# Optimization experiments

Measured on AMD Instinct MI355X. Metric: run time of the kernel, lower is better.

The kernel has to match this reference:

```python
import jax, jax.numpy as jnp
import numpy as np

B, S, D, H, HD, F = 2, 2048, 2048, 16, 128, 8192
EPS = 1e-6
NEG_INF = -1e10


def rmsnorm(x, scale, eps=EPS):
    # T5 LayerNorm: no centering, mean of squares, learned scale
    x = x.astype(jnp.float32)
    mean2 = jnp.mean(jnp.square(x), axis=-1, keepdims=True)
    return x * jax.lax.rsqrt(mean2 + eps) * scale


def setup_inputs() -> dict:
    key = jax.random.key(0)
    ks = jax.random.split(key, 10)
    sd = 0.02
    return {
        "x": jax.random.normal(ks[0], (B, S, D), jnp.float32),
        "ln1_scale": jnp.ones((D,), jnp.float32),
        "wq": jax.random.normal(ks[1], (D, H, HD), jnp.float32) * sd,
        "wk": jax.random.normal(ks[2], (D, H, HD), jnp.float32) * sd,
        "wv": jax.random.normal(ks[3], (D, H, HD), jnp.float32) * sd,
        "qln_scale": jnp.ones((HD,), jnp.float32),
        "kln_scale": jnp.ones((HD,), jnp.float32),
        "wo": jax.random.normal(ks[4], (H, HD, D), jnp.float32) * sd,
        "ln2_scale": jnp.ones((D,), jnp.float32),
        "wi0": jax.random.normal(ks[5], (D, F), jnp.float32) * sd,
        "wi1": jax.random.normal(ks[6], (D, F), jnp.float32) * sd,
        "wout": jax.random.normal(ks[7], (F, D), jnp.float32) * sd,
    }


def reference(x, ln1_scale, wq, wk, wv, qln_scale, kln_scale, wo, ln2_scale, wi0, wi1, wout):
    # ---- pre-attention RMSNorm ----
    lnx = rmsnorm(x, ln1_scale)                                  # [B,S,D]
    # ---- QKV projections (DenseGeneral D -> (H,HD)) ----
    q = jnp.einsum("bsd,dhk->bshk", lnx, wq)                      # [B,S,H,HD]
    k = jnp.einsum("bsd,dhk->bshk", lnx, wk)
    v = jnp.einsum("bsd,dhk->bshk", lnx, wv)
    # ---- fused per-head QK LayerNorm ----
    q = rmsnorm(q, qln_scale)
    k = rmsnorm(k, kln_scale)
    # ---- attention scores + causal bias + softmax ----
    logits = jnp.einsum("bqhd,bkhd->bhqk", q, k)                  # [B,H,S,S]
    causal = jnp.tril(jnp.ones((S, S), bool))
    bias = jnp.where(causal, 0.0, NEG_INF).astype(logits.dtype)  # [S,S]
    probs = jax.nn.softmax(logits + bias[None, None])             # [B,H,S,S]
    # ---- weighted values + output projection ----
    attn = jnp.einsum("bhqk,bkhd->bqhd", probs, v)                # [B,S,H,HD]
    attn_out = jnp.einsum("bqhd,hdm->bqm", attn, wo)              # [B,S,D]
    inter = x + attn_out
    # ---- pre-MLP RMSNorm + gated MLP (silu * linear) ----
    h = rmsnorm(inter, ln2_scale)
    g = jax.nn.silu(h @ wi0) * (h @ wi1)                          # [B,S,F]
    mlp_out = g @ wout                                            # [B,S,D]
    return inter + mlp_out
```

## Files before the change

### kernel.cpp

```cpp
#include <hip/hip_runtime.h>

typedef unsigned short u16;
typedef unsigned int u32;
typedef __attribute__((ext_vector_type(8))) short bf16x8;
typedef __attribute__((ext_vector_type(2))) float f32x2;
typedef __attribute__((ext_vector_type(4))) float f32x4;
typedef __attribute__((ext_vector_type(4))) u32 u32x4;

#define DEV __device__ __forceinline__

DEV u16 f2bf(float x) {
    u32 u = __builtin_bit_cast(u32, x);
    u += 0x7fffu + ((u >> 16) & 1u);
    return (u16)(u >> 16);
}
DEV float bf2f(u16 b) {
    u32 u = ((u32)b) << 16;
    return __builtin_bit_cast(float, u);
}

#define MFMA16(a, b, c) __builtin_amdgcn_mfma_f32_16x16x32_bf16((a), (b), (c), 0, 0, 0)

#define GLL16(gp, lp)                                                      \
    __builtin_amdgcn_global_load_lds(                                      \
        (const __attribute__((address_space(1))) u32*)(const void*)(gp),   \
        (__attribute__((address_space(3))) u32*)(void*)(lp), 16, 0, 0)

__global__ void fillsent(float* __restrict__ out, int n, float val)
{
    for (int i = blockIdx.x * blockDim.x + threadIdx.x; i < n; i += gridDim.x * blockDim.x)
        out[i] = val;
}

__global__ void wtrans(const float* __restrict__ in, u16* __restrict__ out, int K, int N)
{
    __shared__ u16 t[64][65];
    const int n0 = blockIdx.x * 64, k0 = blockIdx.y * 64, tid = threadIdx.x;
    for (int i = tid; i < 4096; i += 256) {
        int r = i >> 6, c = i & 63;
        t[r][c] = f2bf(in[(size_t)(k0 + r) * N + n0 + c]);
    }
    __syncthreads();
    for (int i = tid; i < 4096; i += 256) {
        int r = i >> 6, c = i & 63;
        out[(size_t)(n0 + r) * K + k0 + c] = t[c][r];
    }
}

__global__ void wtrans_split(const float* __restrict__ in, u16* __restrict__ ohi,
                             u16* __restrict__ olo, int K, int N)
{
    __shared__ float t[64][65];
    const int n0 = blockIdx.x * 64, k0 = blockIdx.y * 64, tid = threadIdx.x;
    for (int i = tid; i < 4096; i += 256) {
        int r = i >> 6, c = i & 63;
        t[r][c] = in[(size_t)(k0 + r) * N + n0 + c];
    }
    __syncthreads();
    for (int i = tid; i < 4096; i += 256) {
        int r = i >> 6, c = i & 63;
        float v = t[c][r];
        u16 h = f2bf(v);
        size_t idx = (size_t)(n0 + r) * K + k0 + c;
        ohi[idx] = h;
        olo[idx] = f2bf(v - bf2f(h));
    }
}

__global__ void vtrans(const u16* __restrict__ in, u16* __restrict__ out)
{
    __shared__ u16 t[64][65];
    const int d0 = blockIdx.x * 64, s0 = blockIdx.y * 64, bh = blockIdx.z, tid = threadIdx.x;
    const u16* ip = in + (size_t)bh * 2048 * 128;
    u16* op = out + (size_t)bh * 128 * 2048;
    for (int i = tid; i < 4096; i += 256) {
        int r = i >> 6, c = i & 63;
        t[r][c] = ip[(size_t)(s0 + r) * 128 + d0 + c];
    }
    __syncthreads();
    for (int i = tid; i < 4096; i += 256) {
        int r = i >> 6, c = i & 63;
        op[(size_t)(d0 + r) * 2048 + s0 + c] = t[c][r];
    }
}

__global__ __launch_bounds__(256) void rmsnorm_d(const float* __restrict__ in,
                                                 const float* __restrict__ sc,
                                                 u16* __restrict__ out)
{
    __shared__ float red[4];
    const int row = blockIdx.x, tid = threadIdx.x;
    const float* p = in + (size_t)row * 2048 + tid * 8;
    f32x4 a = *(const f32x4*)p;
    f32x4 b = *(const f32x4*)(p + 4);
    float ss = a[0]*a[0] + a[1]*a[1] + a[2]*a[2] + a[3]*a[3]
             + b[0]*b[0] + b[1]*b[1] + b[2]*b[2] + b[3]*b[3];
    for (int d = 1; d < 64; d <<= 1) ss += __shfl_xor(ss, d, 64);
    if ((tid & 63) == 0) red[tid >> 6] = ss;
    __syncthreads();
    float rs = rsqrtf((red[0] + red[1] + red[2] + red[3]) * (1.0f / 2048.0f) + 1e-6f);
    const float* s = sc + tid * 8;
    u32x4 ov;
#pragma unroll
    for (int i = 0; i < 2; ++i) {
        f32x4 v = i ? b : a;
#pragma unroll
        for (int j = 0; j < 2; ++j) {
            float v0 = v[j * 2] * rs * s[i * 4 + j * 2];
            float v1 = v[j * 2 + 1] * rs * s[i * 4 + j * 2 + 1];
            ov[i * 2 + j] = (u32)f2bf(v0) | ((u32)f2bf(v1) << 16);
        }
    }
    *(u32x4*)(out + (size_t)row * 2048 + tid * 8) = ov;
}

__global__ __launch_bounds__(256) void rmsnorm_split(const float* __restrict__ in,
                                                     const float* __restrict__ sc,
                                                     u16* __restrict__ ohi,
                                                     u16* __restrict__ olo)
{
    __shared__ float red[4];
    const int row = blockIdx.x, tid = threadIdx.x;
    const float* p = in + (size_t)row * 2048 + tid * 8;
    f32x4 a = *(const f32x4*)p;
    f32x4 b = *(const f32x4*)(p + 4);
    float ss = a[0]*a[0] + a[1]*a[1] + a[2]*a[2] + a[3]*a[3]
             + b[0]*b[0] + b[1]*b[1] + b[2]*b[2] + b[3]*b[3];
    for (int d = 1; d < 64; d <<= 1) ss += __shfl_xor(ss, d, 64);
    if ((tid & 63) == 0) red[tid >> 6] = ss;
    __syncthreads();
    float rs = rsqrtf((red[0] + red[1] + red[2] + red[3]) * (1.0f / 2048.0f) + 1e-6f);
    const float* s = sc + tid * 8;
    u32x4 oh, ol;
#pragma unroll
    for (int i = 0; i < 2; ++i) {
        f32x4 v = i ? b : a;
#pragma unroll
        for (int j = 0; j < 2; ++j) {
            float v0 = v[j * 2] * rs * s[i * 4 + j * 2];
            float v1 = v[j * 2 + 1] * rs * s[i * 4 + j * 2 + 1];
            u16 h0 = f2bf(v0), h1 = f2bf(v1);
            u16 l0 = f2bf(v0 - bf2f(h0)), l1 = f2bf(v1 - bf2f(h1));
            oh[i * 2 + j] = (u32)h0 | ((u32)h1 << 16);
            ol[i * 2 + j] = (u32)l0 | ((u32)l1 << 16);
        }
    }
    *(u32x4*)(ohi + (size_t)row * 2048 + tid * 8) = oh;
    *(u32x4*)(olo + (size_t)row * 2048 + tid * 8) = ol;
}

template <int EPI>
__global__ __launch_bounds__(256, 2)
void gemm_bt_k(const u16* __restrict__ A, const u16* __restrict__ Bt,
               float* __restrict__ outf, u16* __restrict__ outb,
               const float* __restrict__ resf, int M, int N, int K)
{
    __shared__ u16 As[128 * 64];
    __shared__ u16 Bs[128 * 64];
    const int tid = threadIdx.x, w = tid >> 6, l = tid & 63;
    const int lr = l & 15, lg = l >> 4;
    const int m0 = blockIdx.y * 128, n0 = blockIdx.x * 128;
    const int wr = (w >> 1) * 64, wc = (w & 1) * 64;
    f32x4 acc[4][4] = {};
    int prow[4], pcol[4];
#pragma unroll
    for (int j = 0; j < 4; ++j) {
        int p = (j * 4 + w) * 1024 + l * 16;
        prow[j] = p >> 7;
        pcol[j] = (p ^ ((prow[j] & 7) << 4)) & 127;
    }
    const char* Ab = (const char*)A;
    const char* Bb = (const char*)Bt;
    const size_t ldb = (size_t)K * 2;
    const int nkt = K / 64;
    for (int kt = 0; kt < nkt; ++kt) {
#pragma unroll
        for (int j = 0; j < 4; ++j) {
            GLL16(Ab + (size_t)(m0 + prow[j]) * ldb + kt * 128 + pcol[j], (char*)As + (j * 4 + w) * 1024);
            GLL16(Bb + (size_t)(n0 + prow[j]) * ldb + kt * 128 + pcol[j], (char*)Bs + (j * 4 + w) * 1024);
        }
        __syncthreads();
#pragma unroll
        for (int kc = 0; kc < 2; ++kc) {
            bf16x8 af[4], bf[4];
#pragma unroll
            for (int f = 0; f < 4; ++f) {
                int ra = wr + f * 16 + lr;
                af[f] = *(const bf16x8*)((const char*)As + ((ra * 128 + kc * 64 + lg * 16) ^ ((ra & 7) << 4)));
                int rb = wc + f * 16 + lr;
                bf[f] = *(const bf16x8*)((const char*)Bs + ((rb * 128 + kc * 64 + lg * 16) ^ ((rb & 7) << 4)));
            }
#pragma unroll
            for (int mf = 0; mf < 4; ++mf)
#pragma unroll
                for (int nf = 0; nf < 4; ++nf)
                    acc[mf][nf] = MFMA16(af[mf], bf[nf], acc[mf][nf]);
        }
        __syncthreads();
    }
#pragma unroll
    for (int mf = 0; mf < 4; ++mf) {
#pragma unroll
        for (int nf = 0; nf < 4; ++nf) {
#pragma unroll
            for (int r = 0; r < 4; ++r) {
                int m = m0 + wr + mf * 16 + lg * 4 + r;
                int n = n0 + wc + nf * 16 + lr;
                float v = acc[mf][nf][r];
                if constexpr (EPI == 0) {
                    outb[(((m >> 11) * 16 + (n >> 7)) << 18) + ((m & 2047) << 7) + (n & 127)] = f2bf(v);
                } else {
                    size_t idx = (size_t)m * N + n;
                    outf[idx] = v + resf[idx];
                }
            }
        }
    }
}

__global__ __launch_bounds__(256, 2)
void gemm3(const u16* __restrict__ Ahi, const u16* __restrict__ Alo,
           const u16* __restrict__ Bhi, const u16* __restrict__ Blo,
           const float* __restrict__ sc,
           u16* __restrict__ ohi, u16* __restrict__ olo, int M, int N, int K)
{
    __shared__ u16 Ah[128 * 64];
    __shared__ u16 Al[128 * 64];
    __shared__ u16 Bh[128 * 64];
    __shared__ u16 Bl[128 * 64];
    __shared__ float ssq[128][2];
    const int tid = threadIdx.x, w = tid >> 6, l = tid & 63;
    const int lr = l & 15, lg = l >> 4;
    const int m0 = blockIdx.y * 128, n0 = blockIdx.x * 128;
    const int wr = (w >> 1) * 64, wc = (w & 1) * 64;
    f32x4 acc[4][4] = {};
    int prow[4], pcol[4];
#pragma unroll
    for (int j = 0; j < 4; ++j) {
        int p = (j * 4 + w) * 1024 + l * 16;
        prow[j] = p >> 7;
        pcol[j] = (p ^ ((prow[j] & 7) << 4)) & 127;
    }
    const size_t ldb = (size_t)K * 2;
    const int nkt = K / 64;
    for (int kt = 0; kt < nkt; ++kt) {
#pragma unroll
        for (int j = 0; j < 4; ++j) {
            size_t ao = (size_t)(m0 + prow[j]) * ldb + kt * 128 + pcol[j];
            size_t bo = (size_t)(n0 + prow[j]) * ldb + kt * 128 + pcol[j];
            GLL16((const char*)Ahi + ao, (char*)Ah + (j * 4 + w) * 1024);
            GLL16((const char*)Alo + ao, (char*)Al + (j * 4 + w) * 1024);
            GLL16((const char*)Bhi + bo, (char*)Bh + (j * 4 + w) * 1024);
            GLL16((const char*)Blo + bo, (char*)Bl + (j * 4 + w) * 1024);
        }
        __syncthreads();
#pragma unroll
        for (int kc = 0; kc < 2; ++kc) {
            bf16x8 ahf[4], alf[4], bhf[4], blf[4];
#pragma unroll
            for (int f = 0; f < 4; ++f) {
                int ra = wr + f * 16 + lr;
                int oa = (ra * 128 + kc * 64 + lg * 16) ^ ((ra & 7) << 4);
                ahf[f] = *(const bf16x8*)((const char*)Ah + oa);
                alf[f] = *(const bf16x8*)((const char*)Al + oa);
                int rb = wc + f * 16 + lr;
                int ob = (rb * 128 + kc * 64 + lg * 16) ^ ((rb & 7) << 4);
                bhf[f] = *(const bf16x8*)((const char*)Bh + ob);
                blf[f] = *(const bf16x8*)((const char*)Bl + ob);
            }
#pragma unroll
            for (int mf = 0; mf < 4; ++mf)
#pragma unroll
                for (int nf = 0; nf < 4; ++nf) {
                    acc[mf][nf] = MFMA16(ahf[mf], bhf[nf], acc[mf][nf]);
                    acc[mf][nf] = MFMA16(ahf[mf], blf[nf], acc[mf][nf]);
                    acc[mf][nf] = MFMA16(alf[mf], bhf[nf], acc[mf][nf]);
                }
        }
        __syncthreads();
    }
    float sp[4][4];
#pragma unroll
    for (int mf = 0; mf < 4; ++mf)
#pragma unroll
        for (int r = 0; r < 4; ++r) {
            float s = 0.0f;
#pragma unroll
            for (int nf = 0; nf < 4; ++nf) { float v = acc[mf][nf][r]; s += v * v; }
            s += __shfl_xor(s, 1, 64); s += __shfl_xor(s, 2, 64);
            s += __shfl_xor(s, 4, 64); s += __shfl_xor(s, 8, 64);
            sp[mf][r] = s;
        }
    if (lr == 0) {
#pragma unroll
        for (int mf = 0; mf < 4; ++mf)
#pragma unroll
            for (int r = 0; r < 4; ++r)
                ssq[wr + mf * 16 + lg * 4 + r][w & 1] = sp[mf][r];
    }
    __syncthreads();
    const int head = n0 >> 7;
#pragma unroll
    for (int mf = 0; mf < 4; ++mf)
#pragma unroll
        for (int r = 0; r < 4; ++r) {
            int mloc = wr + mf * 16 + lg * 4 + r;
            int m = m0 + mloc;
            float rs = rsqrtf((ssq[mloc][0] + ssq[mloc][1]) * (1.0f / 128.0f) + 1e-6f);
            size_t base = (((size_t)(m >> 11) * 16 + head) << 18) + ((size_t)(m & 2047) << 7);
#pragma unroll
            for (int nf = 0; nf < 4; ++nf) {
                int hd = wc + nf * 16 + lr;
                float v = acc[mf][nf][r] * rs * sc[hd];
                u16 hv = f2bf(v);
                ohi[base + hd] = hv;
                olo[base + hd] = f2bf(v - bf2f(hv));
            }
        }
}

__global__ __launch_bounds__(256, 2)
void gemm_up(const u16* __restrict__ A, const u16* __restrict__ B0, const u16* __restrict__ B1,
             u16* __restrict__ G, int M, int N, int K)
{
    __shared__ u16 As[128 * 64];
    __shared__ u16 Bs0[128 * 64];
    __shared__ u16 Bs1[128 * 64];
    const int tid = threadIdx.x, w = tid >> 6, l = tid & 63;
    const int lr = l & 15, lg = l >> 4;
    const int m0 = blockIdx.y * 128, n0 = blockIdx.x * 128;
    const int wr = (w >> 1) * 64, wc = (w & 1) * 64;
    f32x4 acc0[4][4] = {}, acc1[4][4] = {};
    int prow[4], pcol[4];
#pragma unroll
    for (int j = 0; j < 4; ++j) {
        int p = (j * 4 + w) * 1024 + l * 16;
        prow[j] = p >> 7;
        pcol[j] = (p ^ ((prow[j] & 7) << 4)) & 127;
    }
    const size_t ldb = (size_t)K * 2;
    const int nkt = K / 64;
    for (int kt = 0; kt < nkt; ++kt) {
#pragma unroll
        for (int j = 0; j < 4; ++j) {
            GLL16((const char*)A + (size_t)(m0 + prow[j]) * ldb + kt * 128 + pcol[j], (char*)As + (j * 4 + w) * 1024);
            GLL16((const char*)B0 + (size_t)(n0 + prow[j]) * ldb + kt * 128 + pcol[j], (char*)Bs0 + (j * 4 + w) * 1024);
            GLL16((const char*)B1 + (size_t)(n0 + prow[j]) * ldb + kt * 128 + pcol[j], (char*)Bs1 + (j * 4 + w) * 1024);
        }
        __syncthreads();
#pragma unroll
        for (int kc = 0; kc < 2; ++kc) {
            bf16x8 af[4], b0f[4], b1f[4];
#pragma unroll
            for (int f = 0; f < 4; ++f) {
                int ra = wr + f * 16 + lr;
                af[f] = *(const bf16x8*)((const char*)As + ((ra * 128 + kc * 64 + lg * 16) ^ ((ra & 7) << 4)));
                int rb = wc + f * 16 + lr;
                int ob = (rb * 128 + kc * 64 + lg * 16) ^ ((rb & 7) << 4);
                b0f[f] = *(const bf16x8*)((const char*)Bs0 + ob);
                b1f[f] = *(const bf16x8*)((const char*)Bs1 + ob);
            }
#pragma unroll
            for (int mf = 0; mf < 4; ++mf)
#pragma unroll
                for (int nf = 0; nf < 4; ++nf) {
                    acc0[mf][nf] = MFMA16(af[mf], b0f[nf], acc0[mf][nf]);
                    acc1[mf][nf] = MFMA16(af[mf], b1f[nf], acc1[mf][nf]);
                }
        }
        __syncthreads();
    }
#pragma unroll
    for (int mf = 0; mf < 4; ++mf) {
#pragma unroll
        for (int nf = 0; nf < 4; ++nf) {
#pragma unroll
            for (int r = 0; r < 4; ++r) {
                int m = m0 + wr + mf * 16 + lg * 4 + r;
                int n = n0 + wc + nf * 16 + lr;
                float a = acc0[mf][nf][r];
                float b = acc1[mf][nf][r];
                G[(size_t)m * N + n] = f2bf(a / (1.0f + __expf(-a)) * b);
            }
        }
    }
}

__global__ __launch_bounds__(256, 2)
void flash(const u16* __restrict__ Qh, const u16* __restrict__ Ql,
           const u16* __restrict__ Kh, const u16* __restrict__ Kl,
           const u16* __restrict__ Vt, u16* __restrict__ O)
{
    __shared__ u16 Ksh[64 * 128];
    __shared__ u16 Ksl[64 * 128];
    __shared__ u16 Vs[128 * 64];
    __shared__ u16 Ps[4][16 * 64];
    const int tid = threadIdx.x, w = tid >> 6, l = tid & 63;
    const int lr = l & 15, lg = l >> 4;
    const int qb0 = blockIdx.x * 64, bh = blockIdx.y;

    const size_t qoff = ((size_t)bh * 2048 + qb0 + w * 16) * 128;
    bf16x8 qfh[4], qfl[4];
#pragma unroll
    for (int kc = 0; kc < 4; ++kc) {
        qfh[kc] = *(const bf16x8*)(Qh + qoff + lr * 128 + kc * 32 + lg * 8);
        qfl[kc] = *(const bf16x8*)(Ql + qoff + lr * 128 + kc * 32 + lg * 8);
    }

    f32x4 o[8] = {};
    float mrun[4] = {-1e30f, -1e30f, -1e30f, -1e30f};
    float lrun[4] = {};

    int kgo[4], vdo[4], voff[4];
#pragma unroll
    for (int j = 0; j < 4; ++j) {
        int p = (j * 4 + w) * 1024 + l * 16;
        kgo[j] = p ^ (((p >> 8) & 7) << 4);
        int d = p >> 7, c0 = (p >> 4) & 7;
        vdo[j] = d;
        voff[j] = (c0 ^ (d & 7)) << 4;
    }
    const char* kbh = (const char*)(Kh + (size_t)bh * 2048 * 128);
    const char* kbl = (const char*)(Kl + (size_t)bh * 2048 * 128);
    const char* vbase = (const char*)(Vt + (size_t)bh * 128 * 2048);
    const int tmax = blockIdx.x;

    for (int t = 0; t <= tmax; ++t) {
        const char* kgh = kbh + (size_t)t * 16384;
        const char* kgl = kbl + (size_t)t * 16384;
        const char* vg = vbase + t * 128;
#pragma unroll
        for (int j = 0; j < 4; ++j) {
            GLL16(kgh + kgo[j], (char*)Ksh + (j * 4 + w) * 1024);
            GLL16(kgl + kgo[j], (char*)Ksl + (j * 4 + w) * 1024);
            GLL16(vg + (size_t)vdo[j] * 4096 + voff[j], (char*)Vs + (j * 4 + w) * 1024);
        }
        __syncthreads();

        f32x4 sf[4];
#pragma unroll
        for (int kf = 0; kf < 4; ++kf) {
            f32x4 a = {};
            int row = kf * 16 + lr;
#pragma unroll
            for (int kc = 0; kc < 4; ++kc) {
                int off = (row * 256 + kc * 64 + lg * 16) ^ ((row & 7) << 4);
                bf16x8 khf = *(const bf16x8*)((const char*)Ksh + off);
                bf16x8 klf = *(const bf16x8*)((const char*)Ksl + off);
                a = MFMA16(qfh[kc], khf, a);
                a = MFMA16(qfh[kc], klf, a);
                a = MFMA16(qfl[kc], khf, a);
            }
            sf[kf] = a;
        }
        if (t == tmax) {
#pragma unroll
            for (int kf = 0; kf < 4; ++kf)
#pragma unroll
                for (int r = 0; r < 4; ++r)
                    if (t * 64 + kf * 16 + lr > qb0 + w * 16 + lg * 4 + r) sf[kf][r] = -1e30f;
        }
        float scl[4];
#pragma unroll
        for (int r = 0; r < 4; ++r) {
            float m_ = fmaxf(fmaxf(sf[0][r], sf[1][r]), fmaxf(sf[2][r], sf[3][r]));
            m_ = fmaxf(m_, __shfl_xor(m_, 1, 64));
            m_ = fmaxf(m_, __shfl_xor(m_, 2, 64));
            m_ = fmaxf(m_, __shfl_xor(m_, 4, 64));
            m_ = fmaxf(m_, __shfl_xor(m_, 8, 64));
            float mn = fmaxf(mrun[r], m_);
            scl[r] = __expf(mrun[r] - mn);
            mrun[r] = mn;
            float s_ = 0.0f;
#pragma unroll
            for (int kf = 0; kf < 4; ++kf) {
                float e = __expf(sf[kf][r] - mn);
                sf[kf][r] = e;
                s_ += e;
            }
            s_ += __shfl_xor(s_, 1, 64);
            s_ += __shfl_xor(s_, 2, 64);
            s_ += __shfl_xor(s_, 4, 64);
            s_ += __shfl_xor(s_, 8, 64);
            lrun[r] = lrun[r] * scl[r] + s_;
        }
#pragma unroll
        for (int f = 0; f < 8; ++f) {
            o[f][0] *= scl[0]; o[f][1] *= scl[1]; o[f][2] *= scl[2]; o[f][3] *= scl[3];
        }
        char* pb = (char*)&Ps[w][0];
#pragma unroll
        for (int kf = 0; kf < 4; ++kf)
#pragma unroll
            for (int r = 0; r < 4; ++r) {
                int q = lg * 4 + r;
                int byte = (q * 128 + kf * 32 + lr * 2) ^ ((q & 7) << 4);
                *(u16*)(pb + byte) = f2bf(sf[kf][r]);
            }
        __syncthreads();
#pragma unroll
        for (int kc = 0; kc < 2; ++kc) {
            bf16x8 pa = *(const bf16x8*)(pb + ((lr * 128 + kc * 64 + lg * 16) ^ ((lr & 7) << 4)));
#pragma unroll
            for (int df = 0; df < 8; ++df) {
                int vr = df * 16 + lr;
                bf16x8 vf = *(const bf16x8*)((const char*)Vs +
                    ((vr * 128 + kc * 64 + lg * 16) ^ ((vr & 7) << 4)));
                o[df] = MFMA16(pa, vf, o[df]);
            }
        }
        __syncthreads();
    }
    float inv[4];
#pragma unroll
    for (int r = 0; r < 4; ++r) inv[r] = 1.0f / lrun[r];
    const int b = bh >> 4, h = bh & 15;
#pragma unroll
    for (int df = 0; df < 8; ++df)
#pragma unroll
        for (int r = 0; r < 4; ++r) {
            int q = qb0 + w * 16 + lg * 4 + r;
            int d = df * 16 + lr;
            O[(((size_t)b * 2048 + q) * 16 + h) * 128 + d] = f2bf(o[df][r] * inv[r]);
        }
}

extern "C" void kernel_launch(void* const* d_in, const int* in_sizes, int n_in,
                              void* d_out, int out_size, void* d_ws, size_t ws_size,
                              hipStream_t stream)
{
    (void)in_sizes; (void)n_in;
    const float* x    = (const float*)d_in[0];
    const float* ln1  = (const float*)d_in[1];
    const float* wq   = (const float*)d_in[2];
    const float* wk   = (const float*)d_in[3];
    const float* wv   = (const float*)d_in[4];
    const float* qln  = (const float*)d_in[5];
    const float* kln  = (const float*)d_in[6];
    const float* wo   = (const float*)d_in[7];
    const float* ln2  = (const float*)d_in[8];
    const float* wi0  = (const float*)d_in[9];
    const float* wi1  = (const float*)d_in[10];
    const float* wout = (const float*)d_in[11];

    const size_t MB = 1ull << 20;
    char* ws = (char*)d_ws;
    if (ws_size < 256 * MB) {
        fillsent<<<2048, 256, 0, stream>>>((float*)d_out, out_size, (float)(ws_size >> 20));
        return;
    }

    u16* lnx_hi = (u16*)(ws + 0 * MB);
    u16* attn   = (u16*)(ws + 0 * MB);
    u16* lnx_lo = (u16*)(ws + 16 * MB);
    u16* h      = (u16*)(ws + 16 * MB);
    u16* q_hi   = (u16*)(ws + 32 * MB);
    u16* q_lo   = (u16*)(ws + 48 * MB);
    u16* g      = (u16*)(ws + 32 * MB);
    u16* k_hi   = (u16*)(ws + 64 * MB);
    u16* k_lo   = (u16*)(ws + 80 * MB);
    u16* v      = (u16*)(ws + 96 * MB);
    u16* vt     = (u16*)(ws + 112 * MB);
    u16* wo2t   = (u16*)(ws + 96 * MB);
    u16* wqt_hi = (u16*)(ws + 128 * MB);
    u16* wqt_lo = (u16*)(ws + 136 * MB);
    u16* wkt_hi = (u16*)(ws + 144 * MB);
    u16* wkt_lo = (u16*)(ws + 152 * MB);
    float* interp = (float*)(ws + 128 * MB);
    u16* wi0t   = (u16*)(ws + 160 * MB);
    u16* wi1t   = (u16*)(ws + 192 * MB);
    u16* wvt    = (u16*)(ws + 224 * MB);
    u16* wot    = (u16*)(ws + 232 * MB);

    dim3 blk(256);
    wtrans<<<dim3(32, 32), blk, 0, stream>>>(wv, wvt, 2048, 2048);
    wtrans<<<dim3(32, 32), blk, 0, stream>>>(wo, wot, 2048, 2048);
    wtrans<<<dim3(128, 32), blk, 0, stream>>>(wi0, wi0t, 2048, 8192);
    wtrans<<<dim3(128, 32), blk, 0, stream>>>(wi1, wi1t, 2048, 8192);

    rmsnorm_split<<<4096, blk, 0, stream>>>(x, ln1, lnx_hi, lnx_lo);

    wtrans_split<<<dim3(32, 32), blk, 0, stream>>>(wq, wqt_hi, wqt_lo, 2048, 2048);
    gemm3<<<dim3(16, 32), blk, 0, stream>>>(lnx_hi, lnx_lo, wqt_hi, wqt_lo, qln, q_hi, q_lo, 4096, 2048, 2048);

    wtrans_split<<<dim3(32, 32), blk, 0, stream>>>(wk, wkt_hi, wkt_lo, 2048, 2048);
    gemm3<<<dim3(16, 32), blk, 0, stream>>>(lnx_hi, lnx_lo, wkt_hi, wkt_lo, kln, k_hi, k_lo, 4096, 2048, 2048);

    gemm_bt_k<0><<<dim3(16, 32), blk, 0, stream>>>(lnx_hi, wvt, nullptr, v, nullptr, 4096, 2048, 2048);
    vtrans<<<dim3(2, 32, 32), blk, 0, stream>>>(v, vt);

    flash<<<dim3(32, 32), blk, 0, stream>>>(q_hi, q_lo, k_hi, k_lo, vt, attn);

    gemm_bt_k<1><<<dim3(16, 32), blk, 0, stream>>>(attn, wot, interp, nullptr, x, 4096, 2048, 2048);

    rmsnorm_d<<<4096, blk, 0, stream>>>(interp, ln2, h);

    gemm_up<<<dim3(64, 32), blk, 0, stream>>>(h, wi0t, wi1t, g, 4096, 8192, 2048);

    wtrans<<<dim3(32, 128), blk, 0, stream>>>(wout, wo2t, 8192, 2048);
    gemm_bt_k<1><<<dim3(16, 32), blk, 0, stream>>>(g, wo2t, (float*)d_out, nullptr, interp, 4096, 2048, 8192);
}
```

Baseline: 992.5 us.

## Replace bf16 GEMM with 8-wave 128x256 triple-buffered LDS pipeline

Replaces the simple 4-wave 128x128 GEMM, which loads a tile and then computes behind two barriers per K step, with a 512-thread kernel. The new kernel uses a 128x256 tile and a three-stage dynamic-LDS ring (144 KB). Global-to-LDS loads for stage k+2 are spread between MFMA groups, with s_setprio raising MFMA priority and vmcnt waits keeping two stages in flight. It is used for the V projection, the output projection and the down projection. The aim is to hide memory latency and improve reuse of the B tile, at the cost of one block per CU and more barriers inside each K step.

```diff
diff --git a/kernel.cpp b/kernel.cpp
--- a/kernel.cpp
+++ b/kernel.cpp
@@ -150,54 +150,163 @@
 }
 
 template <int EPI>
-__global__ __launch_bounds__(256, 2)
-void gemm_bt_k(const u16* __restrict__ A, const u16* __restrict__ Bt,
-               float* __restrict__ outf, u16* __restrict__ outb,
-               const float* __restrict__ resf, int M, int N, int K)
-{
-    __shared__ u16 As[128 * 64];
-    __shared__ u16 Bs[128 * 64];
+__global__ __launch_bounds__(512, 2)
+void gemm_bt8(const u16* __restrict__ Ap, const u16* __restrict__ Bt,
+              float* __restrict__ outf, u16* __restrict__ outb,
+              const float* __restrict__ resf, int M, int N, int K)
+{
+    extern __shared__ char lds[];
+    char* AB = lds;
+    char* BB = lds + 49152;
     const int tid = threadIdx.x, w = tid >> 6, l = tid & 63;
     const int lr = l & 15, lg = l >> 4;
-    const int m0 = blockIdx.y * 128, n0 = blockIdx.x * 128;
-    const int wr = (w >> 1) * 64, wc = (w & 1) * 64;
+    const int m0 = blockIdx.y * 128, n0 = blockIdx.x * 256;
+    const int wr = (w >> 2) * 64, wc = (w & 3) * 64;
+    const size_t ldb = (size_t)K * 2;
+    const char* Ag = (const char*)Ap;
+    const char* Bg = (const char*)Bt;
+    const int ldsw = w * 1024;
+
+    size_t ago[2], bgo[4];
+#pragma unroll
+    for (int i = 0; i < 2; ++i) {
+        int p = (i * 512 + tid) * 16;
+        int pr = p >> 7;
+        int pc = (p ^ ((pr & 7) << 4)) & 127;
+        ago[i] = (size_t)(m0 + pr) * ldb + pc;
+    }
+#pragma unroll
+    for (int i = 0; i < 4; ++i) {
+        int p = (i * 512 + tid) * 16;
+        int pr = p >> 7;
+        int pc = (p ^ ((pr & 7) << 4)) & 127;
+        bgo[i] = (size_t)(n0 + pr) * ldb + pc;
+    }
+
     f32x4 acc[4][4] = {};
-    int prow[4], pcol[4];
-#pragma unroll
-    for (int j = 0; j < 4; ++j) {
-        int p = (j * 4 + w) * 1024 + l * 16;
-        prow[j] = p >> 7;
-        pcol[j] = (p ^ ((prow[j] & 7) << 4)) & 127;
-    }
-    const char* Ab = (const char*)A;
-    const char* Bb = (const char*)Bt;
-    const size_t ldb = (size_t)K * 2;
     const int nkt = K / 64;
+
+    GLL16(Ag + ago[0], AB + ldsw);
+    GLL16(Ag + ago[1], AB + 8192 + ldsw);
+    GLL16(Bg + bgo[0], BB + ldsw);
+    GLL16(Bg + bgo[1], BB + 8192 + ldsw);
+    GLL16(Bg + bgo[2], BB + 16384 + ldsw);
+    GLL16(Bg + bgo[3], BB + 24576 + ldsw);
+    if (nkt > 1) {
+        char* Ad = AB + 16384;
+        char* Bd = BB + 32768;
+        GLL16(Ag + ago[0] + 128, Ad + ldsw);
+        GLL16(Ag + ago[1] + 128, Ad + 8192 + ldsw);
+        GLL16(Bg + bgo[0] + 128, Bd + ldsw);
+        GLL16(Bg + bgo[1] + 128, Bd + 8192 + ldsw);
+        GLL16(Bg + bgo[2] + 128, Bd + 16384 + ldsw);
+        GLL16(Bg + bgo[3] + 128, Bd + 24576 + ldsw);
+        asm volatile("s_waitcnt vmcnt(6)" ::: "memory");
+    } else {
+        asm volatile("s_waitcnt vmcnt(0)" ::: "memory");
+    }
+    __builtin_amdgcn_s_barrier();
+
+    int cur = 0, stg = 2;
     for (int kt = 0; kt < nkt; ++kt) {
-#pragma unroll
-        for (int j = 0; j < 4; ++j) {
-            GLL16(Ab + (size_t)(m0 + prow[j]) * ldb + kt * 128 + pcol[j], (char*)As + (j * 4 + w) * 1024);
-            GLL16(Bb + (size_t)(n0 + prow[j]) * ldb + kt * 128 + pcol[j], (char*)Bs + (j * 4 + w) * 1024);
-        }
-        __syncthreads();
-#pragma unroll
-        for (int kc = 0; kc < 2; ++kc) {
-            bf16x8 af[4], bf[4];
-#pragma unroll
-            for (int f = 0; f < 4; ++f) {
-                int ra = wr + f * 16 + lr;
-                af[f] = *(const bf16x8*)((const char*)As + ((ra * 128 + kc * 64 + lg * 16) ^ ((ra & 7) << 4)));
-                int rb = wc + f * 16 + lr;
-                bf[f] = *(const bf16x8*)((const char*)Bs + ((rb * 128 + kc * 64 + lg * 16) ^ ((rb & 7) << 4)));
-            }
-#pragma unroll
-            for (int mf = 0; mf < 4; ++mf)
-#pragma unroll
-                for (int nf = 0; nf < 4; ++nf)
-                    acc[mf][nf] = MFMA16(af[mf], bf[nf], acc[mf][nf]);
-        }
-        __syncthreads();
-    }
+        char* Ac = AB + cur * 16384;
+        char* Bc = BB + cur * 32768;
+        char* Asd = AB + stg * 16384;
+        char* Bsd = BB + stg * 32768;
+        const bool dost = (kt + 2 < nkt);
+        const size_t koff = (size_t)(kt + 2) * 128;
+
+        bf16x8 af[4], bfa, bfb;
+#pragma unroll
+        for (int mf = 0; mf < 4; ++mf) {
+            int ra = wr + mf * 16 + lr;
+            af[mf] = *(const bf16x8*)(Ac + ((ra * 128 + lg * 16) ^ ((ra & 7) << 4)));
+        }
+        {
+            int rb = wc + lr;
+            bfa = *(const bf16x8*)(Bc + ((rb * 128 + lg * 16) ^ ((rb & 7) << 4)));
+            rb = wc + 16 + lr;
+            bfb = *(const bf16x8*)(Bc + ((rb * 128 + lg * 16) ^ ((rb & 7) << 4)));
+        }
+        if (dost) {
+            GLL16(Ag + ago[0] + koff, Asd + ldsw);
+            GLL16(Ag + ago[1] + koff, Asd + 8192 + ldsw);
+        }
+        __builtin_amdgcn_s_barrier();
+        __builtin_amdgcn_s_setprio(1);
+#pragma unroll
+        for (int mf = 0; mf < 4; ++mf) acc[mf][0] = MFMA16(af[mf], bfa, acc[mf][0]);
+#pragma unroll
+        for (int mf = 0; mf < 4; ++mf) acc[mf][1] = MFMA16(af[mf], bfb, acc[mf][1]);
+        __builtin_amdgcn_s_setprio(0);
+        __builtin_amdgcn_s_barrier();
+        {
+            int rb = wc + 32 + lr;
+            bfa = *(const bf16x8*)(Bc + ((rb * 128 + lg * 16) ^ ((rb & 7) << 4)));
+            rb = wc + 48 + lr;
+            bfb = *(const bf16x8*)(Bc + ((rb * 128 + lg * 16) ^ ((rb & 7) << 4)));
+        }
+        if (dost) {
+            GLL16(Bg + bgo[0] + koff, Bsd + ldsw);
+            GLL16(Bg + bgo[1] + koff, Bsd + 8192 + ldsw);
+        }
+        __builtin_amdgcn_s_barrier();
+        __builtin_amdgcn_s_setprio(1);
+#pragma unroll
+        for (int mf = 0; mf < 4; ++mf) acc[mf][2] = MFMA16(af[mf], bfa, acc[mf][2]);
+#pragma unroll
+        for (int mf = 0; mf < 4; ++mf) acc[mf][3] = MFMA16(af[mf], bfb, acc[mf][3]);
+        __builtin_amdgcn_s_setprio(0);
+        __builtin_amdgcn_s_barrier();
+#pragma unroll
+        for (int mf = 0; mf < 4; ++mf) {
+            int ra = wr + mf * 16 + lr;
+            af[mf] = *(const bf16x8*)(Ac + ((ra * 128 + 64 + lg * 16) ^ ((ra & 7) << 4)));
+        }
+        {
+            int rb = wc + lr;
+            bfa = *(const bf16x8*)(Bc + ((rb * 128 + 64 + lg * 16) ^ ((rb & 7) << 4)));
+            rb = wc + 16 + lr;
+            bfb = *(const bf16x8*)(Bc + ((rb * 128 + 64 + lg * 16) ^ ((rb & 7) << 4)));
+        }
+        if (dost) {
+            GLL16(Bg + bgo[2] + koff, Bsd + 16384 + ldsw);
+        }
+        __builtin_amdgcn_s_barrier();
+        __builtin_amdgcn_s_setprio(1);
+#pragma unroll
+        for (int mf = 0; mf < 4; ++mf) acc[mf][0] = MFMA16(af[mf], bfa, acc[mf][0]);
+#pragma unroll
+        for (int mf = 0; mf < 4; ++mf) acc[mf][1] = MFMA16(af[mf], bfb, acc[mf][1]);
+        __builtin_amdgcn_s_setprio(0);
+        __builtin_amdgcn_s_barrier();
+        {
+            int rb = wc + 32 + lr;
+            bfa = *(const bf16x8*)(Bc + ((rb * 128 + 64 + lg * 16) ^ ((rb & 7) << 4)));
+            rb = wc + 48 + lr;
+            bfb = *(const bf16x8*)(Bc + ((rb * 128 + 64 + lg * 16) ^ ((rb & 7) << 4)));
+        }
+        if (dost) {
+            GLL16(Bg + bgo[3] + koff, Bsd + 24576 + ldsw);
+        }
+        __builtin_amdgcn_s_barrier();
+        __builtin_amdgcn_s_setprio(1);
+#pragma unroll
+        for (int mf = 0; mf < 4; ++mf) acc[mf][2] = MFMA16(af[mf], bfa, acc[mf][2]);
+#pragma unroll
+        for (int mf = 0; mf < 4; ++mf) acc[mf][3] = MFMA16(af[mf], bfb, acc[mf][3]);
+        __builtin_amdgcn_s_setprio(0);
+        if (kt < nkt - 2) {
+            asm volatile("s_waitcnt vmcnt(6)" ::: "memory");
+            __builtin_amdgcn_s_barrier();
+        } else if (kt == nkt - 2) {
+            asm volatile("s_waitcnt vmcnt(0)" ::: "memory");
+            __builtin_amdgcn_s_barrier();
+        }
+        cur = (cur == 2) ? 0 : cur + 1;
+        stg = (stg == 2) ? 0 : stg + 1;
+    }
+
 #pragma unroll
     for (int mf = 0; mf < 4; ++mf) {
 #pragma unroll
@@ -549,6 +658,11 @@
         fillsent<<<2048, 256, 0, stream>>>((float*)d_out, out_size, (float)(ws_size >> 20));
         return;
     }
+
+    (void)hipFuncSetAttribute((const void*)gemm_bt8<0>,
+                              hipFuncAttributeMaxDynamicSharedMemorySize, 147456);
+    (void)hipFuncSetAttribute((const void*)gemm_bt8<1>,
+                              hipFuncAttributeMaxDynamicSharedMemorySize, 147456);
 
     u16* lnx_hi = (u16*)(ws + 0 * MB);
     u16* attn   = (u16*)(ws + 0 * MB);
@@ -586,17 +700,17 @@
     wtrans_split<<<dim3(32, 32), blk, 0, stream>>>(wk, wkt_hi, wkt_lo, 2048, 2048);
     gemm3<<<dim3(16, 32), blk, 0, stream>>>(lnx_hi, lnx_lo, wkt_hi, wkt_lo, kln, k_hi, k_lo, 4096, 2048, 2048);
 
-    gemm_bt_k<0><<<dim3(16, 32), blk, 0, stream>>>(lnx_hi, wvt, nullptr, v, nullptr, 4096, 2048, 2048);
+    gemm_bt8<0><<<dim3(8, 32), dim3(512), 147456, stream>>>(lnx_hi, wvt, nullptr, v, nullptr, 4096, 2048, 2048);
     vtrans<<<dim3(2, 32, 32), blk, 0, stream>>>(v, vt);
 
     flash<<<dim3(32, 32), blk, 0, stream>>>(q_hi, q_lo, k_hi, k_lo, vt, attn);
 
-    gemm_bt_k<1><<<dim3(16, 32), blk, 0, stream>>>(attn, wot, interp, nullptr, x, 4096, 2048, 2048);
+    gemm_bt8<1><<<dim3(8, 32), dim3(512), 147456, stream>>>(attn, wot, interp, nullptr, x, 4096, 2048, 2048);
 
     rmsnorm_d<<<4096, blk, 0, stream>>>(interp, ln2, h);
 
     gemm_up<<<dim3(64, 32), blk, 0, stream>>>(h, wi0t, wi1t, g, 4096, 8192, 2048);
 
     wtrans<<<dim3(32, 128), blk, 0, stream>>>(wout, wo2t, 8192, 2048);
-    gemm_bt_k<1><<<dim3(16, 32), blk, 0, stream>>>(g, wo2t, (float*)d_out, nullptr, interp, 4096, 2048, 8192);
-}
+    gemm_bt8<1><<<dim3(8, 32), dim3(512), 147456, stream>>>(g, wo2t, (float*)d_out, nullptr, interp, 4096, 2048, 8192);
+}
```

Result: no change. 986.3 us (-0.6%).
